# Kernel optimization log

Hardware: AMD Instinct MI355X
Metric: run time of the kernel (lower is better)

## Reference

```python
import jax, jax.numpy as jnp
import numpy as np

TOP_K = 2  # num_experts_per_tok


def setup_inputs() -> dict:
    key = jax.random.key(0)
    k1, k2, k3, k4, k5 = jax.random.split(key, 5)
    T, H, F, E = 2048, 2048, 1024, 8
    hidden_states = jax.random.normal(k1, (T, H), dtype=jnp.float32)
    router_logits = jax.random.normal(k2, (T, E), dtype=jnp.float32)
    s = 1.0 / np.sqrt(H)
    w1 = jax.random.normal(k3, (E, H, F), dtype=jnp.float32) * s  # gate proj
    w3 = jax.random.normal(k4, (E, H, F), dtype=jnp.float32) * s  # up proj
    w2 = jax.random.normal(k5, (E, F, H), dtype=jnp.float32) * (1.0 / np.sqrt(F))  # down proj
    return {"hidden_states": hidden_states, "router_logits": router_logits,
            "w1": w1, "w3": w3, "w2": w2}


def reference(hidden_states, router_logits, w1, w3, w2):
    # Top-K routing: softmax over raw logits, take top-k probs as combine weights
    # (renormalize_topk_logits=False, routed_scaling_factor=None).
    T, E = router_logits.shape
    probs = jax.nn.softmax(router_logits.astype(jnp.float32), axis=-1)  # (T, E)
    topk_w, topk_ids = jax.lax.top_k(probs, TOP_K)                      # (T, K)
    # Scatter combine weights into a dense (T, E) matrix (zeros off top-k).
    combine = jnp.zeros((T, E), dtype=probs.dtype).at[
        jnp.arange(T)[:, None], topk_ids].add(topk_w)                    # (T, E)

    x = hidden_states
    # SwiGLU expert FFN computed per-expert (dense over all tokens, masked by
    # combine weights -> same math as fused dispatch/grouped-GEMM/combine).
    g = jnp.einsum('th,ehf->etf', x, w1)          # (E, T, F) gate
    u = jnp.einsum('th,ehf->etf', x, w3)          # (E, T, F) up
    act = jax.nn.silu(g) * u                      # (E, T, F)
    act = act * combine.T[:, :, None]             # apply combine weight pre-down-proj
    y = jnp.einsum('etf,efh->th', act, w2)        # (T, H) combined over experts
    return y.astype(hidden_states.dtype)
```

## Files before the change

### kernel.cpp

```cpp
#include <hip/hip_runtime.h>
#include <stdint.h>

#define T_TOK 2048
#define HDIM  2048
#define FDIM  1024
#define NEXP  8

#define BM   128
#define BK   64
#define NTHR 256
#define MT_MAX 16
#define BN1  64
#define BN2  128
#define NT1 (FDIM / BN1)
#define NT2 (HDIM / BN2)
#define NK1 (HDIM / BK)
#define NK2 (FDIM / BK)
#define GRID1 (NEXP * MT_MAX * NT1)
#define GRID2 (NEXP * MT_MAX * NT2)

typedef unsigned short u16;
typedef __attribute__((ext_vector_type(16))) float f32x16;
typedef __attribute__((ext_vector_type(8))) short bf16x8;

__device__ __forceinline__ u16 f2bf(float f) {
  uint32_t u = __float_as_uint(f);
  u += 0x7FFFu + ((u >> 16) & 1u);
  return (u16)(u >> 16);
}

__device__ __forceinline__ uint32_t pack2(float lo, float hi) {
  return (uint32_t)f2bf(lo) | ((uint32_t)f2bf(hi) << 16);
}

__device__ __forceinline__ void glds16(const u16* src, u16* dst) {
  __builtin_amdgcn_global_load_lds(
      (const __attribute__((address_space(1))) uint32_t*)src,
      (__attribute__((address_space(3))) uint32_t*)dst, 16, 0, 0);
}

__global__ void route1_kernel(const float* __restrict__ logits,
                              int* __restrict__ tok_e, float* __restrict__ tok_w,
                              int* __restrict__ counts) {
  __shared__ int lcnt[NEXP];
  const int tid = threadIdx.x;
  const int t = blockIdx.x * 256 + tid;
  if (tid < NEXP) lcnt[tid] = 0;
  __syncthreads();
  float l[NEXP];
#pragma unroll
  for (int e = 0; e < NEXP; ++e) l[e] = logits[t * NEXP + e];
  float m = l[0];
#pragma unroll
  for (int e = 1; e < NEXP; ++e) m = fmaxf(m, l[e]);
  float p[NEXP]; float s = 0.f;
#pragma unroll
  for (int e = 0; e < NEXP; ++e) { p[e] = __expf(l[e] - m); s += p[e]; }
  float inv = 1.f / s;
  int i0 = 0; float p0 = p[0];
#pragma unroll
  for (int e = 1; e < NEXP; ++e) if (p[e] > p0) { p0 = p[e]; i0 = e; }
  int i1 = -1; float p1 = -1.f;
#pragma unroll
  for (int e = 0; e < NEXP; ++e) if (e != i0 && p[e] > p1) { p1 = p[e]; i1 = e; }
  tok_e[t] = i0 | (i1 << 8);
  tok_w[t * 2]     = p0 * inv;
  tok_w[t * 2 + 1] = p1 * inv;
  atomicAdd(&lcnt[i0], 1);
  atomicAdd(&lcnt[i1], 1);
  __syncthreads();
  if (tid < NEXP) atomicAdd(&counts[tid], lcnt[tid]);
}

__global__ void route2_kernel(const int* __restrict__ counts,
                              int* __restrict__ offsets, int* __restrict__ cursor) {
  if (threadIdx.x == 0) {
    int s = 0;
    for (int e = 0; e < NEXP; ++e) { offsets[e] = s; cursor[e] = s; s += counts[e]; }
    offsets[NEXP] = s;
  }
}

__global__ void route3_kernel(const int* __restrict__ tok_e, const float* __restrict__ tok_w,
                              int* __restrict__ cursor,
                              int* __restrict__ token_list, float* __restrict__ slot_w) {
  __shared__ int lcnt[NEXP], lbase[NEXP];
  const int tid = threadIdx.x;
  const int t = blockIdx.x * 256 + tid;
  if (tid < NEXP) lcnt[tid] = 0;
  __syncthreads();
  int ee = tok_e[t];
  int e0 = ee & 255, e1 = ee >> 8;
  int li0 = atomicAdd(&lcnt[e0], 1);
  int li1 = atomicAdd(&lcnt[e1], 1);
  __syncthreads();
  if (tid < NEXP) lbase[tid] = atomicAdd(&cursor[tid], lcnt[tid]);
  __syncthreads();
  int s0 = lbase[e0] + li0;
  int s1 = lbase[e1] + li1;
  token_list[s0] = t; slot_w[s0] = tok_w[t * 2];
  token_list[s1] = t; slot_w[s1] = tok_w[t * 2 + 1];
}

__global__ void convert_x_kernel(const float4* __restrict__ x, ushort4* __restrict__ xb) {
  int i = blockIdx.x * 256 + threadIdx.x;
  float4 v = x[i];
  ushort4 o;
  o.x = f2bf(v.x); o.y = f2bf(v.y); o.z = f2bf(v.z); o.w = f2bf(v.w);
  xb[i] = o;
}

__global__ __launch_bounds__(256, 4)
void tconv4_kernel(const float* __restrict__ w1, const float* __restrict__ w3,
                   const float* __restrict__ w2,
                   u16* __restrict__ w1t, u16* __restrict__ w3t, u16* __restrict__ w2t) {
  const int zb = blockIdx.y;
  const int which = zb >> 3;
  const int e = zb & 7;
  const int x = blockIdx.x;
  const float* src; u16* dst; int R, C, ct, kt;
  if (which == 0)      { src = w1; dst = w1t; R = HDIM; C = FDIM; ct = x & 15; kt = x >> 4; }
  else if (which == 1) { src = w3; dst = w3t; R = HDIM; C = FDIM; ct = x & 15; kt = x >> 4; }
  else                 { src = w2; dst = w2t; R = FDIM; C = HDIM; ct = x & 31; kt = x >> 5; }
  const size_t msz = (size_t)HDIM * FDIM;
  src += (size_t)e * msz;
  dst += (size_t)e * msz;
  const int r0 = kt * 256;
  const int c0 = ct * 64;

  __shared__ uint32_t T[4][64 * 33];
  const int t = threadIdx.x;

  const int kp = t >> 3;
  const int cg = t & 7;
  float4 a0[4], a1[4], b0[4], b1[4];
#pragma unroll
  for (int i = 0; i < 4; ++i) {
    const float* s0 = src + (size_t)(r0 + i * 64 + 2 * kp) * C + c0 + cg * 8;
    a0[i] = *(const float4*)(s0);
    a1[i] = *(const float4*)(s0 + 4);
    b0[i] = *(const float4*)(s0 + C);
    b1[i] = *(const float4*)(s0 + C + 4);
  }
#pragma unroll
  for (int i = 0; i < 4; ++i) {
    uint32_t* Ti = T[i];
    Ti[(cg * 8 + 0) * 33 + kp] = pack2(a0[i].x, b0[i].x);
    Ti[(cg * 8 + 1) * 33 + kp] = pack2(a0[i].y, b0[i].y);
    Ti[(cg * 8 + 2) * 33 + kp] = pack2(a0[i].z, b0[i].z);
    Ti[(cg * 8 + 3) * 33 + kp] = pack2(a0[i].w, b0[i].w);
    Ti[(cg * 8 + 4) * 33 + kp] = pack2(a1[i].x, b1[i].x);
    Ti[(cg * 8 + 5) * 33 + kp] = pack2(a1[i].y, b1[i].y);
    Ti[(cg * 8 + 6) * 33 + kp] = pack2(a1[i].z, b1[i].z);
    Ti[(cg * 8 + 7) * 33 + kp] = pack2(a1[i].w, b1[i].w);
  }
  __syncthreads();

  const int f  = t >> 2;
  const int kg = t & 3;
  uint32_t* drow = (uint32_t*)(dst + (size_t)(c0 + f) * R + r0);
#pragma unroll
  for (int i = 0; i < 4; ++i) {
    const uint32_t* Ti = T[i] + f * 33 + kg * 8;
    uint4 q0 = {Ti[0], Ti[1], Ti[2], Ti[3]};
    uint4 q1 = {Ti[4], Ti[5], Ti[6], Ti[7]};
    *(uint4*)(drow + i * 32 + kg * 8)     = q0;
    *(uint4*)(drow + i * 32 + kg * 8 + 4) = q1;
  }
}

__global__ __launch_bounds__(NTHR, 3)
void gemm1_kernel(const u16* __restrict__ Xb,
                  const u16* __restrict__ w1t,
                  const u16* __restrict__ w3t,
                  const int* __restrict__ token_list,
                  const float* __restrict__ slot_w,
                  const int* __restrict__ counts,
                  const int* __restrict__ offsets,
                  u16* __restrict__ act) {
  const int bid = blockIdx.x;
  const int e  = bid >> 8;
  const int mt = (bid >> 4) & 15;
  const int nt = bid & 15;
  const int cnt = counts[e];
  if (mt * BM >= cnt) return;
  const int off = offsets[e];
  const int tid  = threadIdx.x;
  const int lane = tid & 63;
  const int wid  = tid >> 6;
  const int wr = wid >> 1;
  const int wc = wid & 1;

  __shared__ u16 A_lds[BM * BK];
  __shared__ u16 B1_lds[BN1 * BK];
  __shared__ u16 B3_lds[BN1 * BK];

  const u16* a_src[4];
#pragma unroll
  for (int i = 0; i < 4; ++i) {
    int row = (wid * 4 + i) * 8 + (lane >> 3);
    int mg = mt * BM + row;
    int mc = (mg < cnt) ? mg : (cnt - 1);
    int tok = token_list[off + mc];
    a_src[i] = Xb + (size_t)tok * HDIM + (((lane & 7) ^ (row & 7)) * 8);
  }
  const u16* b1_src[2];
  const u16* b3_src[2];
#pragma unroll
  for (int i = 0; i < 2; ++i) {
    int n = (wid * 2 + i) * 8 + (lane >> 3);
    size_t rowoff = ((size_t)e * FDIM + nt * BN1 + n) * HDIM + (((lane & 7) ^ (n & 7)) * 8);
    b1_src[i] = w1t + rowoff;
    b3_src[i] = w3t + rowoff;
  }

  f32x16 accg[2] = {};
  f32x16 accu[2] = {};

#pragma unroll
  for (int i = 0; i < 4; ++i) glds16(a_src[i], &A_lds[(wid * 4 + i) * 512]);
#pragma unroll
  for (int i = 0; i < 2; ++i) {
    glds16(b1_src[i], &B1_lds[(wid * 2 + i) * 512]);
    glds16(b3_src[i], &B3_lds[(wid * 2 + i) * 512]);
  }

#pragma unroll 1
  for (int t = 0; t < NK1; ++t) {
    __syncthreads();
    bf16x8 af[2][4], bg[4], bu[4];
#pragma unroll
    for (int m = 0; m < 2; ++m) {
      int R = wr * 64 + m * 32 + (lane & 31);
#pragma unroll
      for (int kk = 0; kk < 4; ++kk) {
        int gl = kk * 2 + (lane >> 5);
        af[m][kk] = *(const bf16x8*)&A_lds[R * BK + ((gl ^ (R & 7)) * 8)];
      }
    }
    {
      int R = wc * 32 + (lane & 31);
#pragma unroll
      for (int kk = 0; kk < 4; ++kk) {
        int gl = kk * 2 + (lane >> 5);
        int pos = R * BK + ((gl ^ (R & 7)) * 8);
        bg[kk] = *(const bf16x8*)&B1_lds[pos];
        bu[kk] = *(const bf16x8*)&B3_lds[pos];
      }
    }
    __syncthreads();
    if (t + 1 < NK1) {
      const int ks = (t + 1) * BK;
#pragma unroll
      for (int i = 0; i < 4; ++i) glds16(a_src[i] + ks, &A_lds[(wid * 4 + i) * 512]);
#pragma unroll
      for (int i = 0; i < 2; ++i) {
        glds16(b1_src[i] + ks, &B1_lds[(wid * 2 + i) * 512]);
        glds16(b3_src[i] + ks, &B3_lds[(wid * 2 + i) * 512]);
      }
    }
#pragma unroll
    for (int m = 0; m < 2; ++m)
#pragma unroll
      for (int kk = 0; kk < 4; ++kk) {
        accg[m] = __builtin_amdgcn_mfma_f32_32x32x16_bf16(af[m][kk], bg[kk], accg[m], 0, 0, 0);
        accu[m] = __builtin_amdgcn_mfma_f32_32x32x16_bf16(af[m][kk], bu[kk], accu[m], 0, 0, 0);
      }
  }

  const int fcol = nt * BN1 + wc * 32 + (lane & 31);
#pragma unroll
  for (int m = 0; m < 2; ++m) {
    int base = mt * BM + wr * 64 + m * 32 + 4 * (lane >> 5);
#pragma unroll
    for (int reg = 0; reg < 16; ++reg) {
      int mg = base + (reg & 3) + 8 * (reg >> 2);
      if (mg < cnt) {
        int slot = off + mg;
        float wgt = slot_w[slot];
        float g = accg[m][reg];
        float u = accu[m][reg];
        float sv = g / (1.f + __expf(-g));
        act[(size_t)slot * FDIM + fcol] = f2bf(sv * u * wgt);
      }
    }
  }
}

__global__ __launch_bounds__(NTHR, 3)
void gemm2_kernel(const u16* __restrict__ act,
                  const u16* __restrict__ w2t,
                  const int* __restrict__ token_list,
                  const int* __restrict__ counts,
                  const int* __restrict__ offsets,
                  float* __restrict__ y) {
  const int bid = blockIdx.x;
  const int e  = bid >> 8;
  const int mt = (bid >> 4) & 15;
  const int nt = bid & 15;
  const int cnt = counts[e];
  if (mt * BM >= cnt) return;
  const int off = offsets[e];
  const int tid  = threadIdx.x;
  const int lane = tid & 63;
  const int wid  = tid >> 6;
  const int wr = wid >> 1;
  const int wc = wid & 1;

  __shared__ u16 A_lds[BM * BK];
  __shared__ u16 B_lds[BN2 * BK];

  const u16* a_src[4];
  const u16* b_src[4];
#pragma unroll
  for (int i = 0; i < 4; ++i) {
    int row = (wid * 4 + i) * 8 + (lane >> 3);
    int mg = mt * BM + row;
    int mc = (mg < cnt) ? mg : (cnt - 1);
    a_src[i] = act + (size_t)(off + mc) * FDIM + (((lane & 7) ^ (row & 7)) * 8);
    b_src[i] = w2t + ((size_t)e * HDIM + nt * BN2 + row) * FDIM + (((lane & 7) ^ (row & 7)) * 8);
  }

  f32x16 acc[2][2] = {};

#pragma unroll
  for (int i = 0; i < 4; ++i) {
    glds16(a_src[i], &A_lds[(wid * 4 + i) * 512]);
    glds16(b_src[i], &B_lds[(wid * 4 + i) * 512]);
  }

#pragma unroll 1
  for (int t = 0; t < NK2; ++t) {
    __syncthreads();
    bf16x8 af[2][4], bb[2][4];
#pragma unroll
    for (int m = 0; m < 2; ++m) {
      int R = wr * 64 + m * 32 + (lane & 31);
#pragma unroll
      for (int kk = 0; kk < 4; ++kk) {
        int gl = kk * 2 + (lane >> 5);
        af[m][kk] = *(const bf16x8*)&A_lds[R * BK + ((gl ^ (R & 7)) * 8)];
      }
    }
#pragma unroll
    for (int n = 0; n < 2; ++n) {
      int R = wc * 64 + n * 32 + (lane & 31);
#pragma unroll
      for (int kk = 0; kk < 4; ++kk) {
        int gl = kk * 2 + (lane >> 5);
        bb[n][kk] = *(const bf16x8*)&B_lds[R * BK + ((gl ^ (R & 7)) * 8)];
      }
    }
    __syncthreads();
    if (t + 1 < NK2) {
      const int ks = (t + 1) * BK;
#pragma unroll
      for (int i = 0; i < 4; ++i) {
        glds16(a_src[i] + ks, &A_lds[(wid * 4 + i) * 512]);
        glds16(b_src[i] + ks, &B_lds[(wid * 4 + i) * 512]);
      }
    }
#pragma unroll
    for (int kk = 0; kk < 4; ++kk)
#pragma unroll
      for (int m = 0; m < 2; ++m)
#pragma unroll
        for (int n = 0; n < 2; ++n)
          acc[m][n] = __builtin_amdgcn_mfma_f32_32x32x16_bf16(af[m][kk], bb[n][kk], acc[m][n], 0, 0, 0);
  }

#pragma unroll
  for (int m = 0; m < 2; ++m) {
    int base = mt * BM + wr * 64 + m * 32 + 4 * (lane >> 5);
#pragma unroll
    for (int reg = 0; reg < 16; ++reg) {
      int mg = base + (reg & 3) + 8 * (reg >> 2);
      if (mg < cnt) {
        int slot = off + mg;
        int tok = token_list[slot];
#pragma unroll
        for (int n = 0; n < 2; ++n) {
          int hcol = nt * BN2 + wc * 64 + n * 32 + (lane & 31);
          unsafeAtomicAdd(y + (size_t)tok * HDIM + hcol, acc[m][n][reg]);
        }
      }
    }
  }
}

extern "C" void kernel_launch(void* const* d_in, const int* in_sizes, int n_in,
                              void* d_out, int out_size, void* d_ws, size_t ws_size,
                              hipStream_t stream) {
  (void)in_sizes; (void)n_in; (void)out_size; (void)ws_size;
  const float* hs     = (const float*)d_in[0];
  const float* logits = (const float*)d_in[1];
  const float* w1     = (const float*)d_in[2];
  const float* w3     = (const float*)d_in[3];
  const float* w2     = (const float*)d_in[4];
  float* y = (float*)d_out;

  uint8_t* ws = (uint8_t*)d_ws;
  int*   token_list = (int*)(ws);
  float* slot_w     = (float*)(ws + (16 << 10));
  int*   counts     = (int*)(ws + (32 << 10));
  int*   offsets    = (int*)(ws + (32 << 10) + 128);
  int*   cursor     = (int*)(ws + (32 << 10) + 256);
  int*   tok_e      = (int*)(ws + (33 << 10));
  float* tok_w      = (float*)(ws + (42 << 10));
  const size_t MB = 1 << 20;
  u16*   Xb  = (u16*)(ws + (64 << 10));
  u16*   act = (u16*)(ws + (64 << 10) + 8 * MB);
  u16*   w1t = (u16*)(ws + (64 << 10) + 16 * MB);
  u16*   w3t = (u16*)(ws + (64 << 10) + 48 * MB);
  u16*   w2t = (u16*)(ws + (64 << 10) + 80 * MB);

  hipMemsetAsync(counts, 0, NEXP * sizeof(int), stream);
  route1_kernel<<<T_TOK / 256, 256, 0, stream>>>(logits, tok_e, tok_w, counts);
  route2_kernel<<<1, 64, 0, stream>>>(counts, offsets, cursor);
  route3_kernel<<<T_TOK / 256, 256, 0, stream>>>(tok_e, tok_w, cursor, token_list, slot_w);
  convert_x_kernel<<<(T_TOK * HDIM / 4) / 256, 256, 0, stream>>>((const float4*)hs, (ushort4*)Xb);
  tconv4_kernel<<<dim3(128, 24), 256, 0, stream>>>(w1, w3, w2, w1t, w3t, w2t);
  hipMemsetAsync(d_out, 0, (size_t)T_TOK * HDIM * sizeof(float), stream);
  gemm1_kernel<<<GRID1, NTHR, 0, stream>>>(Xb, w1t, w3t, token_list, slot_w, counts, offsets, act);
  gemm2_kernel<<<GRID2, NTHR, 0, stream>>>(act, w2t, token_list, counts, offsets, y);
}
```

Baseline: 186.1 us.

## Store converted weights as pre-swizzled contiguous 64x64 tiles

The weight transpose-convert kernel now writes bf16 weights into contiguous 8 KB tiles (64 N rows x 64 K), already XOR-swizzled to match the LDS layout, ordered by N-tile then K-step. The GEMM kernels load each B tile as one contiguous block per K step instead of 64 strided rows. This is meant to improve DRAM/cache locality and coalescing of the B loads, and to simplify address math. The GEMM loop structure is unchanged, so the cost of the convert kernel stays about the same.

```diff
diff --git a/kernel.cpp b/kernel.cpp
--- a/kernel.cpp
+++ b/kernel.cpp
@@ -18,6 +18,7 @@
 #define NK2 (FDIM / BK)
 #define GRID1 (NEXP * MT_MAX * NT1)
 #define GRID2 (NEXP * MT_MAX * NT2)
+#define TILE_E 4096
 
 typedef unsigned short u16;
 typedef __attribute__((ext_vector_type(16))) float f32x16;
@@ -111,21 +112,22 @@
 }
 
 __global__ __launch_bounds__(256, 4)
-void tconv4_kernel(const float* __restrict__ w1, const float* __restrict__ w3,
-                   const float* __restrict__ w2,
-                   u16* __restrict__ w1t, u16* __restrict__ w3t, u16* __restrict__ w2t) {
+void tconv_tiled_kernel(const float* __restrict__ w1, const float* __restrict__ w3,
+                        const float* __restrict__ w2,
+                        u16* __restrict__ w1b, u16* __restrict__ w3b, u16* __restrict__ w2b) {
   const int zb = blockIdx.y;
   const int which = zb >> 3;
   const int e = zb & 7;
   const int x = blockIdx.x;
-  const float* src; u16* dst; int R, C, ct, kt;
-  if (which == 0)      { src = w1; dst = w1t; R = HDIM; C = FDIM; ct = x & 15; kt = x >> 4; }
-  else if (which == 1) { src = w3; dst = w3t; R = HDIM; C = FDIM; ct = x & 15; kt = x >> 4; }
-  else                 { src = w2; dst = w2t; R = FDIM; C = HDIM; ct = x & 31; kt = x >> 5; }
+  const float* src; u16* dstbase; int C, ct, ktg, NKT;
+  if (which == 0)      { src = w1; dstbase = w1b; C = FDIM; ct = x & 15; ktg = x >> 4; NKT = 32; }
+  else if (which == 1) { src = w3; dstbase = w3b; C = FDIM; ct = x & 15; ktg = x >> 4; NKT = 32; }
+  else                 { src = w2; dstbase = w2b; C = HDIM; ct = x & 31; ktg = x >> 5; NKT = 16; }
   const size_t msz = (size_t)HDIM * FDIM;
   src += (size_t)e * msz;
-  dst += (size_t)e * msz;
-  const int r0 = kt * 256;
+  const int NTt = (which == 2) ? 32 : 16;
+  u16* blob = dstbase + (((size_t)e * NTt + ct) * NKT + ktg * 4) * TILE_E;
+  const int r0 = ktg * 256;
   const int c0 = ct * 64;
 
   __shared__ uint32_t T[4][64 * 33];
@@ -158,21 +160,23 @@
 
   const int f  = t >> 2;
   const int kg = t & 3;
-  uint32_t* drow = (uint32_t*)(dst + (size_t)(c0 + f) * R + r0);
+  const int swl = f & 7;
+  uint32_t* bu = (uint32_t*)blob;
 #pragma unroll
   for (int i = 0; i < 4; ++i) {
     const uint32_t* Ti = T[i] + f * 33 + kg * 8;
     uint4 q0 = {Ti[0], Ti[1], Ti[2], Ti[3]};
     uint4 q1 = {Ti[4], Ti[5], Ti[6], Ti[7]};
-    *(uint4*)(drow + i * 32 + kg * 8)     = q0;
-    *(uint4*)(drow + i * 32 + kg * 8 + 4) = q1;
+    uint32_t* br = bu + i * 2048 + f * 32;
+    *(uint4*)(br + (((kg * 2) ^ swl) * 4))     = q0;
+    *(uint4*)(br + (((kg * 2 + 1) ^ swl) * 4)) = q1;
   }
 }
 
 __global__ __launch_bounds__(NTHR, 3)
 void gemm1_kernel(const u16* __restrict__ Xb,
-                  const u16* __restrict__ w1t,
-                  const u16* __restrict__ w3t,
+                  const u16* __restrict__ w1b,
+                  const u16* __restrict__ w3b,
                   const int* __restrict__ token_list,
                   const float* __restrict__ slot_w,
                   const int* __restrict__ counts,
@@ -206,12 +210,14 @@
   }
   const u16* b1_src[2];
   const u16* b3_src[2];
-#pragma unroll
-  for (int i = 0; i < 2; ++i) {
-    int n = (wid * 2 + i) * 8 + (lane >> 3);
-    size_t rowoff = ((size_t)e * FDIM + nt * BN1 + n) * HDIM + (((lane & 7) ^ (n & 7)) * 8);
-    b1_src[i] = w1t + rowoff;
-    b3_src[i] = w3t + rowoff;
+  {
+    size_t tbase = ((size_t)(e * 16 + nt) * 32) * TILE_E;
+#pragma unroll
+    for (int i = 0; i < 2; ++i) {
+      int c = wid * 2 + i;
+      b1_src[i] = w1b + tbase + c * 512 + lane * 8;
+      b3_src[i] = w3b + tbase + c * 512 + lane * 8;
+    }
   }
 
   f32x16 accg[2] = {};
@@ -250,13 +256,14 @@
     }
     __syncthreads();
     if (t + 1 < NK1) {
-      const int ks = (t + 1) * BK;
+      const size_t ks = (size_t)(t + 1) * BK;
+      const size_t kb = (size_t)(t + 1) * TILE_E;
 #pragma unroll
       for (int i = 0; i < 4; ++i) glds16(a_src[i] + ks, &A_lds[(wid * 4 + i) * 512]);
 #pragma unroll
       for (int i = 0; i < 2; ++i) {
-        glds16(b1_src[i] + ks, &B1_lds[(wid * 2 + i) * 512]);
-        glds16(b3_src[i] + ks, &B3_lds[(wid * 2 + i) * 512]);
+        glds16(b1_src[i] + kb, &B1_lds[(wid * 2 + i) * 512]);
+        glds16(b3_src[i] + kb, &B3_lds[(wid * 2 + i) * 512]);
       }
     }
 #pragma unroll
@@ -289,7 +296,7 @@
 
 __global__ __launch_bounds__(NTHR, 3)
 void gemm2_kernel(const u16* __restrict__ act,
-                  const u16* __restrict__ w2t,
+                  const u16* __restrict__ w2b,
                   const int* __restrict__ token_list,
                   const int* __restrict__ counts,
                   const int* __restrict__ offsets,
@@ -318,7 +325,9 @@
     int mg = mt * BM + row;
     int mc = (mg < cnt) ? mg : (cnt - 1);
     a_src[i] = act + (size_t)(off + mc) * FDIM + (((lane & 7) ^ (row & 7)) * 8);
-    b_src[i] = w2t + ((size_t)e * HDIM + nt * BN2 + row) * FDIM + (((lane & 7) ^ (row & 7)) * 8);
+    int c = wid * 4 + i;
+    size_t tbase = ((size_t)(e * 32 + nt * 2 + (c >> 3)) * 16) * TILE_E;
+    b_src[i] = w2b + tbase + (c & 7) * 512 + lane * 8;
   }
 
   f32x16 acc[2][2] = {};
@@ -353,11 +362,12 @@
     }
     __syncthreads();
     if (t + 1 < NK2) {
-      const int ks = (t + 1) * BK;
+      const size_t ks = (size_t)(t + 1) * BK;
+      const size_t kb = (size_t)(t + 1) * TILE_E;
 #pragma unroll
       for (int i = 0; i < 4; ++i) {
         glds16(a_src[i] + ks, &A_lds[(wid * 4 + i) * 512]);
-        glds16(b_src[i] + ks, &B_lds[(wid * 4 + i) * 512]);
+        glds16(b_src[i] + kb, &B_lds[(wid * 4 + i) * 512]);
       }
     }
 #pragma unroll
@@ -410,17 +420,17 @@
   const size_t MB = 1 << 20;
   u16*   Xb  = (u16*)(ws + (64 << 10));
   u16*   act = (u16*)(ws + (64 << 10) + 8 * MB);
-  u16*   w1t = (u16*)(ws + (64 << 10) + 16 * MB);
-  u16*   w3t = (u16*)(ws + (64 << 10) + 48 * MB);
-  u16*   w2t = (u16*)(ws + (64 << 10) + 80 * MB);
+  u16*   w1b = (u16*)(ws + (64 << 10) + 16 * MB);
+  u16*   w3b = (u16*)(ws + (64 << 10) + 48 * MB);
+  u16*   w2b = (u16*)(ws + (64 << 10) + 80 * MB);
 
   hipMemsetAsync(counts, 0, NEXP * sizeof(int), stream);
   route1_kernel<<<T_TOK / 256, 256, 0, stream>>>(logits, tok_e, tok_w, counts);
   route2_kernel<<<1, 64, 0, stream>>>(counts, offsets, cursor);
   route3_kernel<<<T_TOK / 256, 256, 0, stream>>>(tok_e, tok_w, cursor, token_list, slot_w);
   convert_x_kernel<<<(T_TOK * HDIM / 4) / 256, 256, 0, stream>>>((const float4*)hs, (ushort4*)Xb);
-  tconv4_kernel<<<dim3(128, 24), 256, 0, stream>>>(w1, w3, w2, w1t, w3t, w2t);
+  tconv_tiled_kernel<<<dim3(128, 24), 256, 0, stream>>>(w1, w3, w2, w1b, w3b, w2b);
   hipMemsetAsync(d_out, 0, (size_t)T_TOK * HDIM * sizeof(float), stream);
-  gemm1_kernel<<<GRID1, NTHR, 0, stream>>>(Xb, w1t, w3t, token_list, slot_w, counts, offsets, act);
-  gemm2_kernel<<<GRID2, NTHR, 0, stream>>>(act, w2t, token_list, counts, offsets, y);
-}
+  gemm1_kernel<<<GRID1, NTHR, 0, stream>>>(Xb, w1b, w3b, token_list, slot_w, counts, offsets, act);
+  gemm2_kernel<<<GRID2, NTHR, 0, stream>>>(act, w2b, token_list, counts, offsets, y);
+}
```

Result: faster. 182.0 us (-2.2%).
